# Kernel tuning notes

Hardware: AMD Instinct MI355X
Metric: run time of the kernel (lower is better)

The kernel has to match this reference:

```python
import jax, jax.numpy as jnp
import numpy as np

B, S, D, H = 8, 2048, 768, 768

def setup_inputs() -> dict:
    key = jax.random.key(0)
    ks = jax.random.split(key, 8)
    s = 1.0 / np.sqrt(D)
    return {
        "x": jax.random.normal(ks[0], (B, S, D), dtype=jnp.float32),
        "y": jax.random.normal(ks[1], (B, S, D), dtype=jnp.float32),
        "Wq": jax.random.uniform(ks[2], (D, H), jnp.float32, -s, s),
        "bq": jax.random.uniform(ks[3], (H,), jnp.float32, -s, s),
        "Wk": jax.random.uniform(ks[4], (D, H), jnp.float32, -s, s),
        "bk": jax.random.uniform(ks[5], (H,), jnp.float32, -s, s),
        "Wv": jax.random.uniform(ks[6], (D, H), jnp.float32, -s, s),
        "bv": jax.random.uniform(ks[7], (H,), jnp.float32, -s, s),
    }

def reference(x, y, Wq, bq, Wk, bk, Wv, bv):
    q = jnp.einsum('bsd,dh->bsh', x, Wq) + bq      # [B,S,H]
    k = jnp.einsum('bsd,dh->bsh', x, Wk) + bk      # [B,S,H]
    v = jnp.einsum('bsd,dh->bsh', y, Wv) + bv      # [B,S,H]
    scores = jnp.einsum('bqh,bkh->bqk', q, k)      # [B,S,S], no scaling in original
    probs = jax.nn.softmax(scores, axis=-1)
    bilinear_v = q * v                              # elementwise gate
    context = jnp.einsum('bqk,bkh->bqh', probs, bilinear_v)
    return context  # dropout is identity in eval mode
```

## Files before the change

kernel.cpp:

```cpp
#include <hip/hip_runtime.h>
#include <cstdint>
#include <cstddef>


#define BM 128
#define BN 128
#define BK 32

using half8 = __attribute__((ext_vector_type(8))) _Float16;
using half4 = __attribute__((ext_vector_type(4))) _Float16;
using f32x4 = __attribute__((ext_vector_type(4))) float;

__global__ __launch_bounds__(256) void cvt2_f32_f16(
    const float* __restrict__ a, const float* __restrict__ b,
    _Float16* __restrict__ oa, _Float16* __restrict__ ob, int n4) {
  const float* in = blockIdx.y ? b : a;
  _Float16* out = blockIdx.y ? ob : oa;
  int i = blockIdx.x * 256 + threadIdx.x;
  if (i >= n4) return;
  float4 v = ((const float4*)in)[i];
  half4 o = {(_Float16)v.x, (_Float16)v.y, (_Float16)v.z, (_Float16)v.w};
  *(half4*)&out[(size_t)i * 4] = o;
}

__global__ __launch_bounds__(256) void tr3_cvt768(
    const float* __restrict__ Wq, const float* __restrict__ Wk,
    const float* __restrict__ Wv, _Float16* __restrict__ Wt) {
  const float* W = (blockIdx.y == 0) ? Wq : (blockIdx.y == 1) ? Wk : Wv;
  _Float16* o = Wt + (size_t)blockIdx.y * 589824;
  int i = blockIdx.x * 256 + threadIdx.x;
  int h = i / 768, d = i - h * 768;
  o[i] = (_Float16)W[d * 768 + h];
}

template <int MODE>
__global__ __launch_bounds__(256) void gemm_bt(
    const _Float16* __restrict__ Ab, int ldA, long sA,
    const _Float16* __restrict__ Bb, int ldB, long sB,
    void* __restrict__ Cb, int ldc, long sC,
    int K, const float* __restrict__ bias, const _Float16* __restrict__ qb,
    const float* __restrict__ bias2, void* __restrict__ Cb2) {
  __shared__ __align__(16) _Float16 lA[BM * BK];
  __shared__ __align__(16) _Float16 lB[BN * BK];

  const int tid  = threadIdx.x;
  const int lane = tid & 63;
  const int quad = lane >> 4;
  const int l15  = lane & 15;
  const int wave = tid >> 6;
  const int wm = (wave >> 1) * 64;
  const int wn = (wave & 1) * 64;
  const long bm = (long)blockIdx.x * BM;
  const long bn = (long)blockIdx.y * BN;
  const _Float16* A = Ab + (long)blockIdx.z * sA;
  const _Float16* B = Bb + (long)blockIdx.z * sB;

  f32x4 acc[4][4] = {};

  const int c0 = tid,        r0 = c0 >> 2, k0c = (c0 & 3) * 8;
  const int c1 = 256 + tid,  r1 = c1 >> 2, k1c = (c1 & 3) * 8;
  const _Float16* gA0 = A + (size_t)(bm + r0) * ldA + k0c;
  const _Float16* gA1 = A + (size_t)(bm + r1) * ldA + k1c;
  const _Float16* gB0 = B + (size_t)(bn + r0) * ldB + k0c;
  const _Float16* gB1 = B + (size_t)(bn + r1) * ldB + k1c;

  for (int kk = 0; kk < K; kk += BK) {
    __syncthreads();
    __builtin_amdgcn_global_load_lds(
        (const __attribute__((address_space(1))) void*)(gA0 + kk),
        (__attribute__((address_space(3))) void*)&lA[c0 * 8], 16, 0, 0);
    __builtin_amdgcn_global_load_lds(
        (const __attribute__((address_space(1))) void*)(gA1 + kk),
        (__attribute__((address_space(3))) void*)&lA[c1 * 8], 16, 0, 0);
    __builtin_amdgcn_global_load_lds(
        (const __attribute__((address_space(1))) void*)(gB0 + kk),
        (__attribute__((address_space(3))) void*)&lB[c0 * 8], 16, 0, 0);
    __builtin_amdgcn_global_load_lds(
        (const __attribute__((address_space(1))) void*)(gB1 + kk),
        (__attribute__((address_space(3))) void*)&lB[c1 * 8], 16, 0, 0);
    __syncthreads();

    half8 af[4], bfr[4];
#pragma unroll
    for (int i = 0; i < 4; i++) {
      af[i]  = *(const half8*)&lA[(wm + i * 16 + l15) * BK + quad * 8];
      bfr[i] = *(const half8*)&lB[(wn + i * 16 + l15) * BK + quad * 8];
    }
#pragma unroll
    for (int i = 0; i < 4; i++)
#pragma unroll
      for (int j = 0; j < 4; j++)
        acc[i][j] = __builtin_amdgcn_mfma_f32_16x16x32_f16(
            af[i], bfr[j], acc[i][j], 0, 0, 0);
  }

  if constexpr (MODE == 1) {
    __shared__ __align__(16) _Float16 xp[4 * 32 * 72];
    _Float16* xw = &xp[wave * 2304];
    const long sbase = (bm & 2047) + wm;
    const long bb = bm >> 11;
    const long hbase = bn + wn;
#pragma unroll
    for (int jh = 0; jh < 2; jh++) {
      __syncthreads();
#pragma unroll
      for (int j2 = 0; j2 < 2; j2++) {
        const int j = jh * 2 + j2;
        const long n_g = hbase + j * 16 + l15;
        const float bsv = bias[n_g];
#pragma unroll
        for (int i = 0; i < 4; i++) {
          half4 pk;
#pragma unroll
          for (int r = 0; r < 4; r++) {
            long m_g = bm + wm + i * 16 + quad * 4 + r;
            float v = acc[i][j][r] + bsv;
            float q = (float)qb[m_g * (long)ldc + n_g];
            pk[r] = (_Float16)(v * q);
          }
          *(half4*)&xw[(j2 * 16 + l15) * 72 + i * 16 + quad * 4] = pk;
        }
      }
      __syncthreads();
#pragma unroll
      for (int t = 0; t < 4; t++) {
        const int n_r = t * 8 + (lane >> 3);
        const int m8 = (lane & 7) * 8;
        half8 vv = *(const half8*)&xw[n_r * 72 + m8];
        *(half8*)&((_Float16*)Cb)[(bb * 768 + hbase + 32 * jh + n_r) * 2048 +
                                  sbase + m8] = vv;
      }
    }
  } else {
#pragma unroll
    for (int i = 0; i < 4; i++) {
#pragma unroll
      for (int j = 0; j < 4; j++) {
#pragma unroll
        for (int r = 0; r < 4; r++) {
          long m = bm + wm + i * 16 + quad * 4 + r;
          long n = bn + wn + j * 16 + l15;
          float v = acc[i][j][r];
          if constexpr (MODE == 3) {
            const bool isq = (bn < 768);
            long nn = isq ? n : n - 768;
            v += (isq ? bias : bias2)[nn];
            _Float16* dst = (_Float16*)(isq ? Cb : Cb2);
            dst[m * ldc + nn] = (_Float16)v;
          } else {
            ((float*)Cb + (long)blockIdx.z * sC)[m * ldc + n] = v;
          }
        }
      }
    }
  }
}

__global__ __launch_bounds__(256) void softmax_rows(
    const float* __restrict__ sc, _Float16* __restrict__ pr, int prPitch) {
  const int row = blockIdx.x;
  const float* x = sc + (size_t)row * 2048;
  const int t = threadIdx.x;
  float4 v0 = ((const float4*)x)[2 * t];
  float4 v1 = ((const float4*)x)[2 * t + 1];
  float e[8] = {v0.x, v0.y, v0.z, v0.w, v1.x, v1.y, v1.z, v1.w};

  float m = e[0];
#pragma unroll
  for (int i = 1; i < 8; i++) m = fmaxf(m, e[i]);
#pragma unroll
  for (int o = 32; o; o >>= 1) m = fmaxf(m, __shfl_xor(m, o, 64));
  __shared__ float red[4];
  if ((t & 63) == 0) red[t >> 6] = m;
  __syncthreads();
  m = fmaxf(fmaxf(red[0], red[1]), fmaxf(red[2], red[3]));

  float s = 0.f;
#pragma unroll
  for (int i = 0; i < 8; i++) { e[i] = __expf(e[i] - m); s += e[i]; }
#pragma unroll
  for (int o = 32; o; o >>= 1) s += __shfl_xor(s, o, 64);
  __syncthreads();
  if ((t & 63) == 0) red[t >> 6] = s;
  __syncthreads();
  s = red[0] + red[1] + red[2] + red[3];
  float inv = 1.0f / s;

  union { _Float16 h[8]; uint4 v; } o;
#pragma unroll
  for (int i = 0; i < 8; i++) o.h[i] = (_Float16)(e[i] * inv);
  ((uint4*)(pr + (size_t)row * prPitch))[t] = o.v;
}

extern "C" void kernel_launch(void* const* d_in, const int* in_sizes, int n_in,
                              void* d_out, int out_size, void* d_ws, size_t ws_size,
                              hipStream_t stream) {
  const float* x  = (const float*)d_in[0];
  const float* y  = (const float*)d_in[1];
  const float* Wq = (const float*)d_in[2];
  const float* bq = (const float*)d_in[3];
  const float* Wk = (const float*)d_in[4];
  const float* bk = (const float*)d_in[5];
  const float* Wv = (const float*)d_in[6];
  const float* bv = (const float*)d_in[7];
  float* out = (float*)d_out;

  const int S = 2048, D = 768, H = 768;
  const long SH = (long)S * H;
  char* ws = (char*)d_ws;
  _Float16* qb  = (_Float16*)(ws + 0);
  _Float16* kb  = (_Float16*)(ws + 25165824);
  _Float16* gT  = (_Float16*)(ws + 50331648);
  _Float16* xb  = (_Float16*)(ws + 75497472);
  _Float16* yb  = (_Float16*)(ws + 100663296);
  _Float16* WtQ = (_Float16*)(ws + 125829120);
  _Float16* WtV = WtQ + 2 * 589824;
  float* scores = (float*)(ws + 75497472);

  cvt2_f32_f16<<<dim3(12288, 2), 256, 0, stream>>>(x, y, xb, yb, 3145728);
  tr3_cvt768<<<dim3(2304, 3), 256, 0, stream>>>(Wq, Wk, Wv, WtQ);

  gemm_bt<3><<<dim3(128, 12, 1), 256, 0, stream>>>(
      xb, D, 0, WtQ, D, 0, qb, H, 0, D, bq, nullptr, bk, kb);
  gemm_bt<1><<<dim3(128, 6, 1), 256, 0, stream>>>(
      yb, D, 0, WtV, D, 0, gT, H, 0, D, bv, qb, nullptr, nullptr);

  _Float16* probs = (_Float16*)scores;
  if (ws_size >= 209715200ull) {
    gemm_bt<2><<<dim3(16, 16, 8), 256, 0, stream>>>(
        qb, H, SH, kb, H, SH, scores, S, (long)S * S, H,
        nullptr, nullptr, nullptr, nullptr);
    softmax_rows<<<16384, 256, 0, stream>>>(scores, probs, 4096);
    gemm_bt<2><<<dim3(16, 6, 8), 256, 0, stream>>>(
        probs, 4096, (long)S * 4096, gT, S, SH, out, H, SH, S,
        nullptr, nullptr, nullptr, nullptr);
  } else {
    for (int r = 0; r < 4; r++) {
      const long b0 = 2 * r;
      gemm_bt<2><<<dim3(16, 16, 2), 256, 0, stream>>>(
          qb + b0 * SH, H, SH, kb + b0 * SH, H, SH, scores, S, (long)S * S, H,
          nullptr, nullptr, nullptr, nullptr);
      softmax_rows<<<4096, 256, 0, stream>>>(scores, probs, 4096);
      gemm_bt<2><<<dim3(16, 6, 2), 256, 0, stream>>>(
          probs, 4096, (long)S * 4096, gT + b0 * SH, S, SH,
          out + b0 * SH, H, SH, S, nullptr, nullptr, nullptr, nullptr);
    }
  }
}
```

Baseline: 448.8 us.

## Add 256x256-tile async-LDS MFMA GEMM for score and context matmuls

```diff
diff --git a/kernel.cpp b/kernel.cpp
--- a/kernel.cpp
+++ b/kernel.cpp
@@ -156,6 +156,124 @@
   }
 }
 
+__global__ __launch_bounds__(512, 2) void gemm256(
+    const _Float16* __restrict__ Ab, int ldA, long sA,
+    const _Float16* __restrict__ Bb, int ldB, long sB,
+    float* __restrict__ Cb, int ldc, long sC, int K) {
+  __shared__ __align__(16) _Float16 lds[8][8192];
+
+  const int tid  = threadIdx.x;
+  const int lane = tid & 63;
+  const int l15  = lane & 15;
+  const int quad = lane >> 4;
+  const int wave = tid >> 6;
+  const int wmi  = wave >> 2;
+  const int wni  = wave & 3;
+
+  const int cpx = gridDim.x >> 3;
+  const int l   = blockIdx.x;
+  const int nl  = (l & 7) * cpx + (l >> 3);
+  const long bm = (long)(nl & 7) * 256;
+  const long bn = (long)(nl >> 3) * 256;
+
+  const _Float16* A = Ab + (long)blockIdx.y * sA;
+  const _Float16* B = Bb + (long)blockIdx.y * sB;
+  float* C = Cb + (long)blockIdx.y * sC;
+
+  const int srow = tid >> 3;
+  const int scol = ((tid & 7) ^ (srow & 7)) * 8;
+  const _Float16* gA = A + (bm + srow) * (long)ldA + scol;
+  const _Float16* gB = B + (bn + srow) * (long)ldB + scol;
+
+#define STAGE(op, GP, LD, buf, half, kt)                                       \
+  { const _Float16* s0_ = (GP) + (long)(half) * 128 * (LD) + (long)(kt) * 64;  \
+    _Float16* d0_ = &lds[(buf) * 4 + (op) * 2 + (half)][tid * 8];              \
+    __builtin_amdgcn_global_load_lds(                                          \
+        (const __attribute__((address_space(1))) void*)s0_,                    \
+        (__attribute__((address_space(3))) void*)d0_, 16, 0, 0);               \
+    __builtin_amdgcn_global_load_lds(                                          \
+        (const __attribute__((address_space(1))) void*)(s0_ + 64 * (long)(LD)),\
+        (__attribute__((address_space(3))) void*)(d0_ + 4096), 16, 0, 0); }
+
+  const int NT = K >> 6;
+  f32x4 acc[8][4] = {};
+
+  STAGE(1, gB, ldB, 0, 0, 0)
+  STAGE(1, gB, ldB, 0, 1, 0)
+  STAGE(0, gA, ldA, 0, 0, 0)
+  STAGE(0, gA, ldA, 0, 1, 0)
+  STAGE(1, gB, ldB, 1, 0, 1)
+  STAGE(1, gB, ldB, 1, 1, 1)
+  asm volatile("s_waitcnt vmcnt(4)" ::: "memory");
+  __builtin_amdgcn_s_barrier();
+  asm volatile("" ::: "memory");
+
+  const int sw4 = (l15 & 7) << 4;
+  const int rB0 = (wni & 1) * 64;
+  half8 bf[4][2];
+
+  for (int kt = 0; kt < NT; ++kt) {
+    const int b = kt & 1;
+    const char* lA = (const char*)lds[b * 4 + wmi];
+    const char* lB = (const char*)lds[b * 4 + 2 + (wni >> 1)];
+#pragma unroll
+    for (int ph = 0; ph < 4; ++ph) {
+      half8 af[2][2];
+#pragma unroll
+      for (int i2 = 0; i2 < 2; ++i2)
+#pragma unroll
+        for (int ks = 0; ks < 2; ++ks)
+          af[i2][ks] = *(const half8*)(lA + (((ph * 2 + i2) * 16 + l15) * 128 +
+                                             ((((ks << 2) | quad) << 4) ^ sw4)));
+      if (ph == 0) {
+#pragma unroll
+        for (int j = 0; j < 4; ++j)
+#pragma unroll
+          for (int ks = 0; ks < 2; ++ks)
+            bf[j][ks] = *(const half8*)(lB + ((rB0 + j * 16 + l15) * 128 +
+                                              ((((ks << 2) | quad) << 4) ^ sw4)));
+      }
+      if (ph == 0 && kt + 1 < NT) STAGE(0, gA, ldA, b ^ 1, 0, kt + 1)
+      if (ph == 1 && kt + 1 < NT) STAGE(0, gA, ldA, b ^ 1, 1, kt + 1)
+      if (ph == 2 && kt + 2 < NT) STAGE(1, gB, ldB, b, 0, kt + 2)
+      if (ph == 3 && kt + 2 < NT) STAGE(1, gB, ldB, b, 1, kt + 2)
+      asm volatile("" ::: "memory");
+      __builtin_amdgcn_s_barrier();
+      asm volatile("" ::: "memory");
+      __builtin_amdgcn_s_setprio(1);
+#pragma unroll
+      for (int i2 = 0; i2 < 2; ++i2)
+#pragma unroll
+        for (int j = 0; j < 4; ++j)
+#pragma unroll
+          for (int ks = 0; ks < 2; ++ks)
+            acc[ph * 2 + i2][j] = __builtin_amdgcn_mfma_f32_16x16x32_f16(
+                af[i2][ks], bf[j][ks], acc[ph * 2 + i2][j], 0, 0, 0);
+      __builtin_amdgcn_s_setprio(0);
+      if (ph == 3) {
+        if (kt < NT - 2) {
+          asm volatile("s_waitcnt vmcnt(4)" ::: "memory");
+        } else if (kt == NT - 2) {
+          asm volatile("s_waitcnt vmcnt(0)" ::: "memory");
+        }
+      }
+      asm volatile("" ::: "memory");
+      __builtin_amdgcn_s_barrier();
+      asm volatile("" ::: "memory");
+    }
+  }
+#undef STAGE
+
+  float* Cp = C + (bm + wmi * 128 + quad * 4) * (long)ldc + bn + wni * 64 + l15;
+#pragma unroll
+  for (int i = 0; i < 8; ++i)
+#pragma unroll
+    for (int j = 0; j < 4; ++j)
+#pragma unroll
+      for (int r = 0; r < 4; ++r)
+        Cp[(i * 16 + r) * (long)ldc + j * 16] = acc[i][j][r];
+}
+
 __global__ __launch_bounds__(256) void softmax_rows(
     const float* __restrict__ sc, _Float16* __restrict__ pr, int prPitch) {
   const int row = blockIdx.x;
@@ -227,23 +345,20 @@
 
   _Float16* probs = (_Float16*)scores;
   if (ws_size >= 209715200ull) {
-    gemm_bt<2><<<dim3(16, 16, 8), 256, 0, stream>>>(
-        qb, H, SH, kb, H, SH, scores, S, (long)S * S, H,
-        nullptr, nullptr, nullptr, nullptr);
+    gemm256<<<dim3(64, 8), 512, 0, stream>>>(
+        qb, H, SH, kb, H, SH, scores, S, (long)S * S, D);
     softmax_rows<<<16384, 256, 0, stream>>>(scores, probs, 4096);
-    gemm_bt<2><<<dim3(16, 6, 8), 256, 0, stream>>>(
-        probs, 4096, (long)S * 4096, gT, S, SH, out, H, SH, S,
-        nullptr, nullptr, nullptr, nullptr);
+    gemm256<<<dim3(24, 8), 512, 0, stream>>>(
+        probs, 4096, (long)S * 4096, gT, S, SH, out, H, SH, S);
   } else {
     for (int r = 0; r < 4; r++) {
       const long b0 = 2 * r;
-      gemm_bt<2><<<dim3(16, 16, 2), 256, 0, stream>>>(
-          qb + b0 * SH, H, SH, kb + b0 * SH, H, SH, scores, S, (long)S * S, H,
-          nullptr, nullptr, nullptr, nullptr);
+      gemm256<<<dim3(64, 2), 512, 0, stream>>>(
+          qb + b0 * SH, H, SH, kb + b0 * SH, H, SH, scores, S, (long)S * S, D);
       softmax_rows<<<4096, 256, 0, stream>>>(scores, probs, 4096);
-      gemm_bt<2><<<dim3(16, 6, 2), 256, 0, stream>>>(
+      gemm256<<<dim3(24, 2), 512, 0, stream>>>(
           probs, 4096, (long)S * 4096, gT + b0 * SH, S, SH,
-          out + b0 * SH, H, SH, S, nullptr, nullptr, nullptr, nullptr);
+          out + b0 * SH, H, SH, S);
     }
   }
 }
```

Measured after the change: 409.7 us. 1.1x faster.
